# Performance work log

Measured on AMD Instinct MI355X. Metric: run time of the kernel, lower is better.

The kernel has to match this reference:

```python
import jax, jax.numpy as jnp
import numpy as np

V, D, K = 400000, 300, 10

def setup_inputs() -> dict:
    key = jax.random.key(0)
    k1, k2 = jax.random.split(key)
    word2vec = jax.random.normal(k1, (V, D), dtype=jnp.float32)  # embedding table
    w = jax.random.normal(k2, (D,), dtype=jnp.float32)           # query vector
    return {"word2vec": word2vec, "w": w, "k": K}

def reference(word2vec, w, k):
    # cosine similarity: (word2vec @ w) / (||rows|| * ||w||), matching torch eps placement
    dots = word2vec @ w                                          # [V]
    row_norms = jnp.sqrt(jnp.sum(word2vec * word2vec, axis=1) + 1e-9)  # [V]
    q_norm = jnp.sqrt(jnp.sum(w * w))
    cos = dots / (row_norms * q_norm)                            # [V]
    vals, topk = jax.lax.top_k(cos, k)                           # top-k neighbors
    return vals, topk
```

## Files before the change

kernel.cpp:

```cpp
#include <hip/hip_runtime.h>

#define D    300
#define NF4  75
#define K    10
#define WPB  4
#define GPB  16
#define NBLOCKS 2048
#define NGROUPS (NBLOCKS * GPB)

#define P2_BLOCKS  64
#define P2_THREADS 1024
#define P2_CPT     7

typedef float f32x4 __attribute__((ext_vector_type(4)));

__device__ __forceinline__ f32x4 ntload(const f32x4* p) {
    return __builtin_nontemporal_load(p);
}

__device__ __forceinline__ float d4(f32x4 a, f32x4 b) {
    return a[0]*b[0] + a[1]*b[1] + a[2]*b[2] + a[3]*b[3];
}

#define RED16(x) { x += __shfl_xor(x, 8, 64); x += __shfl_xor(x, 4, 64); \
                   x += __shfl_xor(x, 2, 64); x += __shfl_xor(x, 1, 64); }

__global__ __launch_bounds__(256) void cos_all(
    const float* __restrict__ emb, const float* __restrict__ wvec,
    float* __restrict__ score, int V, int s)
{
    const int tid  = threadIdx.x;
    const int lane = tid & 63;
    const int wid  = tid >> 6;
    const int l16  = lane & 15;
    const int rg   = lane >> 4;
    const bool tl  = (l16 < NF4 - 64);

    const f32x4* w4p = (const f32x4*)wvec;
    f32x4 w0 = w4p[l16];
    f32x4 w1 = w4p[l16 + 16];
    f32x4 w2 = w4p[l16 + 32];
    f32x4 w3 = w4p[l16 + 48];
    f32x4 w4t = 0.f;
    if (tl) w4t = w4p[l16 + 64];

    float qsq = d4(w0,w0)+d4(w1,w1)+d4(w2,w2)+d4(w3,w3)+d4(w4t,w4t);
    RED16(qsq);
    const float qn = sqrtf(qsq);

    const int g0 = (blockIdx.x * WPB + wid) * 4 + rg;
    const size_t stepF4 = (size_t)s * NF4;

    const f32x4* pA = (const f32x4*)emb + (size_t)g0 * NF4;
    const f32x4* pB = pA + stepF4;

    f32x4 A0,A1,A2,A3,A4, B0,B1,B2,B3,B4;
    A4 = 0.f;
    B4 = 0.f;

#define LOADROW(P, C0,C1,C2,C3,C4) \
    { C0 = ntload((P)+l16);    C1 = ntload((P)+l16+16); \
      C2 = ntload((P)+l16+32); C3 = ntload((P)+l16+48); \
      if (tl) C4 = ntload((P)+l16+64); }

#define DOTSQ(C0,C1,C2,C3,C4, DOT, SQ)                       \
    float DOT, SQ;                                           \
    {   float _da = d4(C0,w0) + d4(C1,w1);                   \
        float _db = d4(C2,w2) + d4(C3,w3) + d4(C4,w4t);      \
        float _sa = d4(C0,C0) + d4(C1,C1);                   \
        float _sb = d4(C2,C2) + d4(C3,C3) + d4(C4,C4);       \
        DOT = _da + _db; SQ = _sa + _sb; }

#define FINISH(DOT, SQ, ROW)                                 \
    { RED16(DOT); RED16(SQ);                                 \
      float _c = DOT / (sqrtf(SQ + 1e-9f) * qn);             \
      if (l16 == 0) score[ROW] = _c; }

    LOADROW(pA, A0,A1,A2,A3,A4);
    LOADROW(pB, B0,B1,B2,B3,B4);

    int rowA = g0;
    int rowB = g0 + s;
    const int nfull = V / s;

    for (int it = 0; it < nfull/2 - 1; ++it) {
        {
            DOTSQ(A0,A1,A2,A3,A4, dA, sA);
            pA += 2*stepF4;
            LOADROW(pA, A0,A1,A2,A3,A4);
            FINISH(dA, sA, rowA);
            rowA += 2*s;
        }
        {
            DOTSQ(B0,B1,B2,B3,B4, dB, sB);
            pB += 2*stepF4;
            LOADROW(pB, B0,B1,B2,B3,B4);
            FINISH(dB, sB, rowB);
            rowB += 2*s;
        }
    }

    {
        DOTSQ(A0,A1,A2,A3,A4, dA, sA);
        const bool hasTail = (rowA + 2*s) < V;
        if (hasTail) { pA += 2*stepF4; LOADROW(pA, A0,A1,A2,A3,A4); }
        FINISH(dA, sA, rowA);
        {
            DOTSQ(B0,B1,B2,B3,B4, dB, sB);
            FINISH(dB, sB, rowB);
        }
        if (hasTail) {
            DOTSQ(A0,A1,A2,A3,A4, dT, sT);
            FINISH(dT, sT, rowA + 2*s);
        }
    }
#undef LOADROW
#undef DOTSQ
#undef FINISH
}

__global__ __launch_bounds__(P2_THREADS) void block_topk(
    const float* __restrict__ score, int V,
    float* __restrict__ cand_v, int* __restrict__ cand_i)
{
    __shared__ float rv[16];
    __shared__ int   rp[16];
    __shared__ int   s_bp;

    const int tid  = threadIdx.x;
    const int lane = tid & 63;
    const int wid  = tid >> 6;
    const int per  = (V + gridDim.x - 1) / gridDim.x;
    const int base = blockIdx.x * per;

    float v[P2_CPT];
    #pragma unroll
    for (int t = 0; t < P2_CPT; ++t) {
        int i = tid + t * P2_THREADS;
        v[t] = (i < per && base + i < V) ? score[base + i] : -3e38f;
    }

    for (int p = 0; p < K; ++p) {
        float bestv = -3e38f; int bestpos = 0x7fffffff;
        #pragma unroll
        for (int t = 0; t < P2_CPT; ++t) {
            if (v[t] > bestv) { bestv = v[t]; bestpos = tid + t * P2_THREADS; }
        }
        #pragma unroll
        for (int m = 32; m >= 1; m >>= 1) {
            float ov = __shfl_xor(bestv, m, 64);
            int   op = __shfl_xor(bestpos, m, 64);
            if (ov > bestv || (ov == bestv && op < bestpos)) { bestv = ov; bestpos = op; }
        }
        if (lane == 0) { rv[wid] = bestv; rp[wid] = bestpos; }
        __syncthreads();
        if (tid == 0) {
            float bv = rv[0]; int bp = rp[0];
            for (int i = 1; i < 16; ++i)
                if (rv[i] > bv || (rv[i] == bv && rp[i] < bp)) { bv = rv[i]; bp = rp[i]; }
            cand_v[blockIdx.x*K + p] = bv;
            cand_i[blockIdx.x*K + p] = base + bp;
            s_bp = bp;
        }
        __syncthreads();
        const int wbp = s_bp;
        #pragma unroll
        for (int t = 0; t < P2_CPT; ++t) {
            if (tid + t * P2_THREADS == wbp) v[t] = -3e38f;
        }
        __syncthreads();
    }
}

__global__ __launch_bounds__(P2_THREADS) void final_topk(
    const float* __restrict__ cand_v, const int* __restrict__ cand_i,
    int nc, float* __restrict__ out)
{
    __shared__ float rv[16];
    __shared__ int   rp[16];
    __shared__ int   s_bp;

    const int tid  = threadIdx.x;
    const int lane = tid & 63;
    const int wid  = tid >> 6;

    float v0 = (tid < nc) ? cand_v[tid] : -3e38f;

    for (int p = 0; p < K; ++p) {
        float bestv = v0; int bestpos = tid;
        #pragma unroll
        for (int m = 32; m >= 1; m >>= 1) {
            float ov = __shfl_xor(bestv, m, 64);
            int   op = __shfl_xor(bestpos, m, 64);
            if (ov > bestv || (ov == bestv && op < bestpos)) { bestv = ov; bestpos = op; }
        }
        if (lane == 0) { rv[wid] = bestv; rp[wid] = bestpos; }
        __syncthreads();
        if (tid == 0) {
            float bv = rv[0]; int bp = rp[0];
            for (int i = 1; i < 16; ++i)
                if (rv[i] > bv || (rv[i] == bv && rp[i] < bp)) { bv = rv[i]; bp = rp[i]; }
            out[p]     = bv;
            out[K + p] = (float)cand_i[bp];
            s_bp = bp;
        }
        __syncthreads();
        if (tid == s_bp) v0 = -3e38f;
        __syncthreads();
    }
}

extern "C" void kernel_launch(void* const* d_in, const int* in_sizes, int n_in,
                              void* d_out, int out_size, void* d_ws, size_t ws_size,
                              hipStream_t stream) {
    const float* emb  = (const float*)d_in[0];
    const float* wvec = (const float*)d_in[1];
    const int V = in_sizes[0] / D;

    float* score  = (float*)d_ws;
    float* cand_v = score + V;
    int*   cand_i = (int*)(cand_v + P2_BLOCKS * K);

    cos_all<<<NBLOCKS, 256, 0, stream>>>(emb, wvec, score, V, NGROUPS);
    block_topk<<<P2_BLOCKS, P2_THREADS, 0, stream>>>(score, V, cand_v, cand_i);
    final_topk<<<1, P2_THREADS, 0, stream>>>(cand_v, cand_i, P2_BLOCKS * K, (float*)d_out);
}
```

Measured before the change: 122.1 us.

## Simplify cosine loop and widen block top-k to more blocks

Replaces the manually double-buffered, software-pipelined row loop in the cosine kernel with a simple strided loop, leaving latency hiding to occupancy and the compiler. Raises the first-stage top-k grid from 64 to 256 blocks with fewer elements per thread, so each block does a shorter serial K-pass selection. The final top-k kernel now handles 2560 candidates with three values per thread. The trade-off is losing explicit load prefetch in the memory-bound pass and adding a larger final reduction.

```diff
diff --git a/kernel.cpp b/kernel.cpp
--- a/kernel.cpp
+++ b/kernel.cpp
@@ -8,9 +8,11 @@
 #define NBLOCKS 2048
 #define NGROUPS (NBLOCKS * GPB)
 
-#define P2_BLOCKS  64
+#define P2_BLOCKS  256
 #define P2_THREADS 1024
-#define P2_CPT     7
+#define P2_CPT     2
+#define NCAND      (P2_BLOCKS * K)
+#define F_CPT      3
 
 typedef float f32x4 __attribute__((ext_vector_type(4)));
 
@@ -51,72 +53,27 @@
     const int g0 = (blockIdx.x * WPB + wid) * 4 + rg;
     const size_t stepF4 = (size_t)s * NF4;
 
-    const f32x4* pA = (const f32x4*)emb + (size_t)g0 * NF4;
-    const f32x4* pB = pA + stepF4;
+    const f32x4* p = (const f32x4*)emb + (size_t)g0 * NF4 + l16;
 
-    f32x4 A0,A1,A2,A3,A4, B0,B1,B2,B3,B4;
-    A4 = 0.f;
-    B4 = 0.f;
+    for (int r = g0; r < V; r += s, p += stepF4) {
+        f32x4 a0 = ntload(p);
+        f32x4 a1 = ntload(p + 16);
+        f32x4 a2 = ntload(p + 32);
+        f32x4 a3 = ntload(p + 48);
+        f32x4 a4 = 0.f;
+        if (tl) a4 = ntload(p + 64);
 
-#define LOADROW(P, C0,C1,C2,C3,C4) \
-    { C0 = ntload((P)+l16);    C1 = ntload((P)+l16+16); \
-      C2 = ntload((P)+l16+32); C3 = ntload((P)+l16+48); \
-      if (tl) C4 = ntload((P)+l16+64); }
+        float da = d4(a0,w0) + d4(a1,w1);
+        float db = d4(a2,w2) + d4(a3,w3) + d4(a4,w4t);
+        float sa = d4(a0,a0) + d4(a1,a1);
+        float sb = d4(a2,a2) + d4(a3,a3) + d4(a4,a4);
+        float dot = da + db;
+        float sq  = sa + sb;
 
-#define DOTSQ(C0,C1,C2,C3,C4, DOT, SQ)                       \
-    float DOT, SQ;                                           \
-    {   float _da = d4(C0,w0) + d4(C1,w1);                   \
-        float _db = d4(C2,w2) + d4(C3,w3) + d4(C4,w4t);      \
-        float _sa = d4(C0,C0) + d4(C1,C1);                   \
-        float _sb = d4(C2,C2) + d4(C3,C3) + d4(C4,C4);       \
-        DOT = _da + _db; SQ = _sa + _sb; }
-
-#define FINISH(DOT, SQ, ROW)                                 \
-    { RED16(DOT); RED16(SQ);                                 \
-      float _c = DOT / (sqrtf(SQ + 1e-9f) * qn);             \
-      if (l16 == 0) score[ROW] = _c; }
-
-    LOADROW(pA, A0,A1,A2,A3,A4);
-    LOADROW(pB, B0,B1,B2,B3,B4);
-
-    int rowA = g0;
-    int rowB = g0 + s;
-    const int nfull = V / s;
-
-    for (int it = 0; it < nfull/2 - 1; ++it) {
-        {
-            DOTSQ(A0,A1,A2,A3,A4, dA, sA);
-            pA += 2*stepF4;
-            LOADROW(pA, A0,A1,A2,A3,A4);
-            FINISH(dA, sA, rowA);
-            rowA += 2*s;
-        }
-        {
-            DOTSQ(B0,B1,B2,B3,B4, dB, sB);
-            pB += 2*stepF4;
-            LOADROW(pB, B0,B1,B2,B3,B4);
-            FINISH(dB, sB, rowB);
-            rowB += 2*s;
-        }
+        RED16(dot); RED16(sq);
+        float c = dot / (sqrtf(sq + 1e-9f) * qn);
+        if (l16 == 0) score[r] = c;
     }
-
-    {
-        DOTSQ(A0,A1,A2,A3,A4, dA, sA);
-        const bool hasTail = (rowA + 2*s) < V;
-        if (hasTail) { pA += 2*stepF4; LOADROW(pA, A0,A1,A2,A3,A4); }
-        FINISH(dA, sA, rowA);
-        {
-            DOTSQ(B0,B1,B2,B3,B4, dB, sB);
-            FINISH(dB, sB, rowB);
-        }
-        if (hasTail) {
-            DOTSQ(A0,A1,A2,A3,A4, dT, sT);
-            FINISH(dT, sT, rowA + 2*s);
-        }
-    }
-#undef LOADROW
-#undef DOTSQ
-#undef FINISH
 }
 
 __global__ __launch_bounds__(P2_THREADS) void block_topk(
@@ -130,7 +87,7 @@
     const int tid  = threadIdx.x;
     const int lane = tid & 63;
     const int wid  = tid >> 6;
-    const int per  = (V + gridDim.x - 1) / gridDim.x;
+    const int per  = (V + P2_BLOCKS - 1) / P2_BLOCKS;
     const int base = blockIdx.x * per;
 
     float v[P2_CPT];
@@ -174,7 +131,7 @@
 
 __global__ __launch_bounds__(P2_THREADS) void final_topk(
     const float* __restrict__ cand_v, const int* __restrict__ cand_i,
-    int nc, float* __restrict__ out)
+    float* __restrict__ out)
 {
     __shared__ float rv[16];
     __shared__ int   rp[16];
@@ -184,10 +141,19 @@
     const int lane = tid & 63;
     const int wid  = tid >> 6;
 
-    float v0 = (tid < nc) ? cand_v[tid] : -3e38f;
+    float v[F_CPT];
+    #pragma unroll
+    for (int t = 0; t < F_CPT; ++t) {
+        int i = tid + t * P2_THREADS;
+        v[t] = (i < NCAND) ? cand_v[i] : -3e38f;
+    }
 
     for (int p = 0; p < K; ++p) {
-        float bestv = v0; int bestpos = tid;
+        float bestv = -3e38f; int bestpos = 0x7fffffff;
+        #pragma unroll
+        for (int t = 0; t < F_CPT; ++t) {
+            if (v[t] > bestv) { bestv = v[t]; bestpos = tid + t * P2_THREADS; }
+        }
         #pragma unroll
         for (int m = 32; m >= 1; m >>= 1) {
             float ov = __shfl_xor(bestv, m, 64);
@@ -205,7 +171,11 @@
             s_bp = bp;
         }
         __syncthreads();
-        if (tid == s_bp) v0 = -3e38f;
+        const int wbp = s_bp;
+        #pragma unroll
+        for (int t = 0; t < F_CPT; ++t) {
+            if (tid + t * P2_THREADS == wbp) v[t] = -3e38f;
+        }
         __syncthreads();
     }
 }
@@ -219,9 +189,9 @@
 
     float* score  = (float*)d_ws;
     float* cand_v = score + V;
-    int*   cand_i = (int*)(cand_v + P2_BLOCKS * K);
+    int*   cand_i = (int*)(cand_v + NCAND);
 
     cos_all<<<NBLOCKS, 256, 0, stream>>>(emb, wvec, score, V, NGROUPS);
     block_topk<<<P2_BLOCKS, P2_THREADS, 0, stream>>>(score, V, cand_v, cand_i);
-    final_topk<<<1, P2_THREADS, 0, stream>>>(cand_v, cand_i, P2_BLOCKS * K, (float*)d_out);
+    final_topk<<<1, P2_THREADS, 0, stream>>>(cand_v, cand_i, (float*)d_out);
 }
```

Result: no change. 122.4 us (+0.2%).
